# Kernel tuning notes

Hardware: AMD Instinct MI355X
Metric: run time of the kernel (lower is better)

## Reference

```python
import math
import jax, jax.numpy as jnp
import numpy as np

N_HEADS = 16


def setup_inputs() -> dict:
    key = jax.random.key(0)
    k1, k2 = jax.random.split(key)
    qkv = jax.random.normal(k1, (2, 3072, 2048), dtype=jnp.float32)
    mask = jax.random.randint(k2, (2, 1, 2048), 0, 2).astype(jnp.bool_)
    return {"qkv": qkv, "mask": mask}


def reference(qkv, mask):
    bs, width, length = qkv.shape
    ch = width // (3 * N_HEADS)
    q, k, v = jnp.split(qkv, 3, axis=1)  # each [bs, H*C, T]
    scale = 1.0 / math.sqrt(math.sqrt(ch))  # applied to both q and k
    q = (q * scale).reshape(bs * N_HEADS, ch, length)
    k = (k * scale).reshape(bs * N_HEADS, ch, length)
    # [B*H, T, T] scores
    weight = jnp.einsum('bct,bcs->bts', q, k)
    # mask: [bs, 1, T] bool, True = valid token
    inv = ~mask[:, 0, :]                      # [bs, T]
    pad = inv[:, None, :] | inv[:, :, None]   # [bs, T, T]
    pad = jnp.broadcast_to(pad[:, None], (bs, N_HEADS, length, length))
    pad = pad.reshape(bs * N_HEADS, length, length)
    weight = jnp.where(pad, jnp.finfo(weight.dtype).min, weight)
    weight = jax.nn.softmax(weight.astype(jnp.float32), axis=-1).astype(qkv.dtype)
    a = jnp.einsum('bts,bcs->bct', weight, v.reshape(bs * N_HEADS, ch, length))
    return a.reshape(bs, N_HEADS * ch, length)
```

## Files before the change

kernel.cpp:

```cpp
#include <hip/hip_runtime.h>
#include <float.h>


typedef __attribute__((ext_vector_type(8))) short bf16x8;
typedef __attribute__((ext_vector_type(4))) float f32x4;

#define TSEQ 2048
#define QT_OFF 0L
#define KF_OFF 4194304L
#define VF_OFF 8388608L

#if __has_builtin(__builtin_amdgcn_exp2f)
#define EXPFN(x) __builtin_amdgcn_exp2f(x)
#define SM_SCALE (0.125f * 1.44269504088896f)
#else
#define EXPFN(x) __expf(x)
#define SM_SCALE 0.125f
#endif

__device__ inline short f2bf(float x) {
    union { float f; unsigned u; } un; un.f = x;
    unsigned r = un.u + 0x7fffu + ((un.u >> 16) & 1u);
    return (short)(r >> 16);
}

__device__ inline unsigned pkbf(float a, float b) {
    unsigned au = __float_as_uint(a) + 0x8000u;
    unsigned bu = __float_as_uint(b) + 0x8000u;
    return __builtin_amdgcn_perm(bu, au, 0x07060302u);
}

__global__ __launch_bounds__(256) void prep_kernel(
    const float* __restrict__ qkv, short* __restrict__ ws)
{
    const int tid = threadIdx.x;
    const int job = blockIdx.x;
    if (job < 2048) {
        __shared__ float Ls[64 * 65];
        const int which = job & 1;
        const int rest  = job >> 1;
        const int bh = rest & 31, tt = rest >> 5;
        const int b = bh >> 4, h = bh & 15;
        const float* src = qkv + (long)b * 6291456 + ((long)(which * 1024 + h * 64)) * TSEQ + tt * 64;
        #pragma unroll
        for (int ch = 0; ch < 4; ++ch) {
            int idx = tid + ch * 256;
            int c = idx >> 4, tch = idx & 15;
            float4 v = *(const float4*)(src + (long)c * TSEQ + tch * 4);
            float* L = &Ls[c * 65 + tch * 4];
            L[0] = v.x; L[1] = v.y; L[2] = v.z; L[3] = v.w;
        }
        __syncthreads();
        if (which == 0) {
            short* dst = ws + QT_OFF + ((long)bh * TSEQ + tt * 64) * 64;
            #pragma unroll
            for (int ch = 0; ch < 2; ++ch) {
                int idx = tid + ch * 256;
                int t = idx >> 3, cch = idx & 7;
                bf16x8 o;
                #pragma unroll
                for (int j = 0; j < 8; ++j)
                    o[j] = f2bf(Ls[(cch * 8 + j) * 65 + t] * SM_SCALE);
                *(bf16x8*)(dst + (long)t * 64 + cch * 8) = o;
            }
        } else {
            short* dst = ws + KF_OFF + (long)(bh * 32 + tt) * 4096;
            #pragma unroll
            for (int ch = 0; ch < 2; ++ch) {
                int u = tid + ch * 256;
                int f = u >> 6, lane = u & 63;
                int q = lane >> 4, l15 = lane & 15;
                int hf = f & 1, ns = f >> 1;
                bf16x8 o;
                #pragma unroll
                for (int j = 0; j < 8; ++j)
                    o[j] = f2bf(Ls[(hf * 32 + q * 8 + j) * 65 + ns * 16 + l15]);
                *(bf16x8*)(dst + f * 512 + lane * 8) = o;
            }
        }
    } else {
        const int v = job - 2048;
        const int head = v >> 5, it = v & 31;
        const int b = head >> 4, h = head & 15;
        short* dst = ws + VF_OFF + (long)(head * 32 + it) * 4096;
        #pragma unroll
        for (int ch = 0; ch < 2; ++ch) {
            int u = tid * 2 + ch;
            int f = u >> 6, lane = u & 63;
            int q = lane >> 4, l15 = lane & 15;
            int hf = f & 1, nc = f >> 1;
            const float* src = qkv + (long)b * 6291456
                + ((long)(2048 + h * 64 + nc * 16 + l15)) * TSEQ
                + it * 64 + hf * 32 + q * 8;
            float4 a  = *(const float4*)src;
            float4 c4 = *(const float4*)(src + 4);
            bf16x8 o;
            o[0] = f2bf(a.x);  o[1] = f2bf(a.y);  o[2] = f2bf(a.z);  o[3] = f2bf(a.w);
            o[4] = f2bf(c4.x); o[5] = f2bf(c4.y); o[6] = f2bf(c4.z); o[7] = f2bf(c4.w);
            *(bf16x8*)(dst + f * 512 + lane * 8) = o;
        }
    }
}

__global__ __launch_bounds__(512, 2) void attn_kernel(
    const short* __restrict__ ws, const int* __restrict__ mask,
    float* __restrict__ out)
{
    __shared__ __align__(16) char smem[66560];
    short* Ps  = (short*)smem;
    float* mbf = (float*)(smem + 32768);
    float* Os  = (float*)smem;

    const int tid  = threadIdx.x;
    const int lane = tid & 63, wid = tid >> 6;
    const int l15  = lane & 15, quad = lane >> 4;

    const int blk  = blockIdx.x;
    const int head = blk & 31;
    const int qt   = blk >> 5;
    const int b    = head >> 4, h = head & 15;
    const int t0   = qt * 256;

    const short* QT = ws + QT_OFF + (long)head * 131072;
    const short* KF = ws + KF_OFF + (long)head * 131072;
    const short* VF = ws + VF_OFF + (long)head * 131072;
    const long obase = ((long)b * 1024 + h * 64) * TSEQ;

    for (int i = tid; i < TSEQ; i += 512)
        mbf[i] = (mask[b * TSEQ + i] != 0) ? 0.0f : -1e30f;
    __syncthreads();

    bf16x8 qb[2][2];
    #pragma unroll
    for (int nt = 0; nt < 2; ++nt)
        #pragma unroll
        for (int hf = 0; hf < 2; ++hf)
            qb[nt][hf] = *(const bf16x8*)(QT +
                (long)(t0 + wid * 32 + nt * 16 + l15) * 64 + quad * 8 + hf * 32);
    bool qv[2];
    #pragma unroll
    for (int nt = 0; nt < 2; ++nt)
        qv[nt] = (mbf[t0 + wid * 32 + nt * 16 + l15] != 0.0f);

    float l_s[2] = {0.0f, 0.0f};
    f32x4 Oacc[2][4];
    #pragma unroll
    for (int mt = 0; mt < 2; ++mt)
        #pragma unroll
        for (int nc = 0; nc < 4; ++nc)
            #pragma unroll
            for (int r = 0; r < 4; ++r) Oacc[mt][nc][r] = 0.0f;

    short* Pw = Ps + wid * 2048;

    bf16x8 kc[8];
    #pragma unroll
    for (int f = 0; f < 8; ++f)
        kc[f] = *(const bf16x8*)(KF + (long)f * 512 + lane * 8);

    for (int it = 0; it < 32; ++it) {
        const int itn = (it + 1) & 31;

        bf16x8 vf[8];
        #pragma unroll
        for (int f = 0; f < 8; ++f)
            vf[f] = *(const bf16x8*)(VF + ((long)it * 8 + f) * 512 + lane * 8);
        bf16x8 kn[8];
        #pragma unroll
        for (int f = 0; f < 8; ++f)
            kn[f] = *(const bf16x8*)(KF + ((long)itn * 8 + f) * 512 + lane * 8);

        f32x4 bias[4];
        #pragma unroll
        for (int ns = 0; ns < 4; ++ns)
            bias[ns] = *(const f32x4*)&mbf[it * 64 + ns * 16 + quad * 4];

        f32x4 Sacc[4][2];
        #pragma unroll
        for (int ns = 0; ns < 4; ++ns)
            #pragma unroll
            for (int nt = 0; nt < 2; ++nt) {
                Sacc[ns][nt] = __builtin_amdgcn_mfma_f32_16x16x32_bf16(
                    kc[ns * 2 + 0], qb[nt][0], bias[ns], 0, 0, 0);
                Sacc[ns][nt] = __builtin_amdgcn_mfma_f32_16x16x32_bf16(
                    kc[ns * 2 + 1], qb[nt][1], Sacc[ns][nt], 0, 0, 0);
            }

        #pragma unroll
        for (int nt = 0; nt < 2; ++nt) {
            const int row = nt * 16 + l15;
            const int sw  = (row & 7) ^ ((row & 8) >> 1);
            float ls = 0.0f;
            #pragma unroll
            for (int ns = 0; ns < 4; ++ns) {
                float pv[4];
                #pragma unroll
                for (int r = 0; r < 4; ++r) {
                    float e = EXPFN(Sacc[ns][nt][r]);
                    pv[r] = qv[nt] ? 1.0f : e;
                    ls += pv[r];
                }
                const int cbp = (ns * 2 + (quad >> 1)) ^ sw;
                uint2 pk;
                pk.x = pkbf(pv[0], pv[1]);
                pk.y = pkbf(pv[2], pv[3]);
                *(uint2*)&Pw[row * 64 + cbp * 8 + (quad & 1) * 4] = pk;
            }
            ls += __shfl_xor(ls, 16);
            ls += __shfl_xor(ls, 32);
            l_s[nt] += ls;
        }

        bf16x8 pa[2][2];
        #pragma unroll
        for (int mt = 0; mt < 2; ++mt) {
            const int row = mt * 16 + l15;
            const int sw  = (row & 7) ^ ((row & 8) >> 1);
            #pragma unroll
            for (int hf = 0; hf < 2; ++hf)
                pa[mt][hf] = *(const bf16x8*)&Pw[row * 64 + ((quad + 4 * hf) ^ sw) * 8];
        }
        #pragma unroll
        for (int hf = 0; hf < 2; ++hf)
            #pragma unroll
            for (int nc = 0; nc < 4; ++nc)
                #pragma unroll
                for (int mt = 0; mt < 2; ++mt)
                    Oacc[mt][nc] = __builtin_amdgcn_mfma_f32_16x16x32_bf16(
                        pa[mt][hf], vf[nc * 2 + hf], Oacc[mt][nc], 0, 0, 0);

        #pragma unroll
        for (int f = 0; f < 8; ++f) kc[f] = kn[f];
    }

    __syncthreads();
    float inv[2];
    #pragma unroll
    for (int nt = 0; nt < 2; ++nt) inv[nt] = 1.0f / l_s[nt];
    float iw[2][4];
    #pragma unroll
    for (int mt = 0; mt < 2; ++mt)
        #pragma unroll
        for (int r = 0; r < 4; ++r)
            iw[mt][r] = __shfl(inv[mt], 4 * quad + r);
    #pragma unroll
    for (int mt = 0; mt < 2; ++mt)
        #pragma unroll
        for (int nc = 0; nc < 4; ++nc) {
            float4 o;
            o.x = Oacc[mt][nc][0] * iw[mt][0];
            o.y = Oacc[mt][nc][1] * iw[mt][1];
            o.z = Oacc[mt][nc][2] * iw[mt][2];
            o.w = Oacc[mt][nc][3] * iw[mt][3];
            *(float4*)&Os[(nc * 16 + l15) * 260 + wid * 32 + mt * 16 + quad * 4] = o;
        }
    __syncthreads();
    #pragma unroll
    for (int ch = 0; ch < 8; ++ch) {
        int idx = tid + ch * 512;
        int c = idx >> 6, tch = idx & 63;
        *(float4*)(out + obase + (long)c * TSEQ + t0 + tch * 4) =
            *(const float4*)&Os[c * 260 + tch * 4];
    }
}

extern "C" void kernel_launch(void* const* d_in, const int* in_sizes, int n_in,
                              void* d_out, int out_size, void* d_ws, size_t ws_size,
                              hipStream_t stream) {
    const float* qkv  = (const float*)d_in[0];
    const int*   mask = (const int*)d_in[1];
    float*       out  = (float*)d_out;
    short*       ws   = (short*)d_ws;
    prep_kernel<<<dim3(3072), dim3(256), 0, stream>>>(qkv, ws);
    attn_kernel<<<dim3(256), dim3(512), 0, stream>>>(ws, mask, out);
}
```

Baseline: 142.7 us.

## Stage K/V tiles in shared double-buffered LDS via global_load_lds

Until now every wave loaded the full K and V tiles for each iteration straight from global memory into registers, so the same data was fetched eight times per block. Now each wave issues one 16-byte global_load_lds per K and V tile into a double-buffered LDS region that all waves share. The next tile is prefetched while the current one is consumed, and waves read their fragments from LDS. MFMA sections are also wrapped in s_setprio to favour matrix issue. The trade-off is a block-wide barrier every iteration and more LDS per block (73728 bytes), which could limit overlap between waves.

```diff
diff --git a/kernel.cpp b/kernel.cpp
--- a/kernel.cpp
+++ b/kernel.cpp
@@ -17,6 +17,10 @@
 #define EXPFN(x) __expf(x)
 #define SM_SCALE 0.125f
 #endif
+
+#define GLOAD16(g, l) __builtin_amdgcn_global_load_lds( \
+    (const __attribute__((address_space(1))) void*)(g), \
+    (__attribute__((address_space(3))) void*)(l), 16, 0, 0)
 
 __device__ inline short f2bf(float x) {
     union { float f; unsigned u; } un; un.f = x;
@@ -106,9 +110,9 @@
     const short* __restrict__ ws, const int* __restrict__ mask,
     float* __restrict__ out)
 {
-    __shared__ __align__(16) char smem[66560];
-    short* Ps  = (short*)smem;
-    float* mbf = (float*)(smem + 32768);
+    __shared__ __align__(16) char smem[73728];
+    short* Ps  = (short*)(smem + 32768);
+    float* mbf = (float*)(smem + 65536);
     float* Os  = (float*)smem;
 
     const int tid  = threadIdx.x;
@@ -122,12 +126,15 @@
     const int t0   = qt * 256;
 
     const short* QT = ws + QT_OFF + (long)head * 131072;
-    const short* KF = ws + KF_OFF + (long)head * 131072;
-    const short* VF = ws + VF_OFF + (long)head * 131072;
+    const char*  KB = (const char*)(ws + KF_OFF + (long)head * 131072);
+    const char*  VB = (const char*)(ws + VF_OFF + (long)head * 131072);
     const long obase = ((long)b * 1024 + h * 64) * TSEQ;
 
     for (int i = tid; i < TSEQ; i += 512)
         mbf[i] = (mask[b * TSEQ + i] != 0) ? 0.0f : -1e30f;
+
+    GLOAD16(KB + wid * 1024 + lane * 16, smem + wid * 1024);
+    GLOAD16(VB + wid * 1024 + lane * 16, smem + 8192 + wid * 1024);
     __syncthreads();
 
     bf16x8 qb[2][2];
@@ -153,22 +160,22 @@
 
     short* Pw = Ps + wid * 2048;
 
-    bf16x8 kc[8];
-    #pragma unroll
-    for (int f = 0; f < 8; ++f)
-        kc[f] = *(const bf16x8*)(KF + (long)f * 512 + lane * 8);
-
+    int cur = 0;
     for (int it = 0; it < 32; ++it) {
-        const int itn = (it + 1) & 31;
-
-        bf16x8 vf[8];
+        if (it != 31) {
+            const long nb = (long)(it + 1) * 8192;
+            GLOAD16(KB + nb + wid * 1024 + lane * 16,
+                    smem + (cur ^ 1) * 16384 + wid * 1024);
+            GLOAD16(VB + nb + wid * 1024 + lane * 16,
+                    smem + (cur ^ 1) * 16384 + 8192 + wid * 1024);
+        }
+        const short* kb = (const short*)(smem + cur * 16384);
+        const short* vb = (const short*)(smem + cur * 16384 + 8192);
+
+        bf16x8 kc[8];
         #pragma unroll
         for (int f = 0; f < 8; ++f)
-            vf[f] = *(const bf16x8*)(VF + ((long)it * 8 + f) * 512 + lane * 8);
-        bf16x8 kn[8];
-        #pragma unroll
-        for (int f = 0; f < 8; ++f)
-            kn[f] = *(const bf16x8*)(KF + ((long)itn * 8 + f) * 512 + lane * 8);
+            kc[f] = *(const bf16x8*)(kb + f * 512 + lane * 8);
 
         f32x4 bias[4];
         #pragma unroll
@@ -176,6 +183,7 @@
             bias[ns] = *(const f32x4*)&mbf[it * 64 + ns * 16 + quad * 4];
 
         f32x4 Sacc[4][2];
+        __builtin_amdgcn_s_setprio(1);
         #pragma unroll
         for (int ns = 0; ns < 4; ++ns)
             #pragma unroll
@@ -185,6 +193,7 @@
                 Sacc[ns][nt] = __builtin_amdgcn_mfma_f32_16x16x32_bf16(
                     kc[ns * 2 + 1], qb[nt][1], Sacc[ns][nt], 0, 0, 0);
             }
+        __builtin_amdgcn_s_setprio(0);
 
         #pragma unroll
         for (int nt = 0; nt < 2; ++nt) {
@@ -220,6 +229,12 @@
             for (int hf = 0; hf < 2; ++hf)
                 pa[mt][hf] = *(const bf16x8*)&Pw[row * 64 + ((quad + 4 * hf) ^ sw) * 8];
         }
+        bf16x8 vf[8];
+        #pragma unroll
+        for (int f = 0; f < 8; ++f)
+            vf[f] = *(const bf16x8*)(vb + f * 512 + lane * 8);
+
+        __builtin_amdgcn_s_setprio(1);
         #pragma unroll
         for (int hf = 0; hf < 2; ++hf)
             #pragma unroll
@@ -228,12 +243,12 @@
                 for (int mt = 0; mt < 2; ++mt)
                     Oacc[mt][nc] = __builtin_amdgcn_mfma_f32_16x16x32_bf16(
                         pa[mt][hf], vf[nc * 2 + hf], Oacc[mt][nc], 0, 0, 0);
-
-        #pragma unroll
-        for (int f = 0; f < 8; ++f) kc[f] = kn[f];
+        __builtin_amdgcn_s_setprio(0);
+
+        __syncthreads();
+        cur ^= 1;
     }
 
-    __syncthreads();
     float inv[2];
     #pragma unroll
     for (int nt = 0; nt < 2; ++nt) inv[nt] = 1.0f / l_s[nt];
```

Result: slower. 148.1 us (+3.8%).

## Split key sequence across wave pairs with smaller query tiles for more blocks

Applied to the files above, without the earlier changes.

The attention kernel now uses 64-query tiles with 256-thread blocks (1024 blocks instead of 256). Each pair of waves processes interleaved halves of the key tiles, and the partial row sums and outputs are combined through shared memory at the end. The K prefetch pipeline is removed, V loads move after the softmax, and s_setprio wraps the MFMA sections. The prep kernel's V write mapping also changes. The aim is better CU occupancy and load balance on a 256-CU part, at the cost of an extra reduction step and less software prefetching.

```diff
diff --git a/kernel.cpp b/kernel.cpp
--- a/kernel.cpp
+++ b/kernel.cpp
@@ -85,7 +85,7 @@
         short* dst = ws + VF_OFF + (long)(head * 32 + it) * 4096;
         #pragma unroll
         for (int ch = 0; ch < 2; ++ch) {
-            int u = tid * 2 + ch;
+            int u = tid + ch * 256;
             int f = u >> 6, lane = u & 63;
             int q = lane >> 4, l15 = lane & 15;
             int hf = f & 1, nc = f >> 1;
@@ -102,31 +102,33 @@
     }
 }
 
-__global__ __launch_bounds__(512, 2) void attn_kernel(
-    const short* __restrict__ ws, const int* __restrict__ mask,
+__global__ __launch_bounds__(256, 4) void attn_kernel(
+    const short* __restrict__ wsp, const int* __restrict__ mask,
     float* __restrict__ out)
 {
-    __shared__ __align__(16) char smem[66560];
+    __shared__ __align__(16) char smem[24576];
     short* Ps  = (short*)smem;
-    float* mbf = (float*)(smem + 32768);
+    float* mbf = (float*)(smem + 16384);
     float* Os  = (float*)smem;
+    float* Lc  = (float*)(smem + 20480);
 
     const int tid  = threadIdx.x;
     const int lane = tid & 63, wid = tid >> 6;
     const int l15  = lane & 15, quad = lane >> 4;
+    const int wq   = wid & 1,  wss  = wid >> 1;
 
     const int blk  = blockIdx.x;
     const int head = blk & 31;
     const int qt   = blk >> 5;
     const int b    = head >> 4, h = head & 15;
-    const int t0   = qt * 256;
-
-    const short* QT = ws + QT_OFF + (long)head * 131072;
-    const short* KF = ws + KF_OFF + (long)head * 131072;
-    const short* VF = ws + VF_OFF + (long)head * 131072;
+    const int t0   = qt * 64;
+
+    const short* QT = wsp + QT_OFF + (long)head * 131072;
+    const short* KF = wsp + KF_OFF + (long)head * 131072;
+    const short* VF = wsp + VF_OFF + (long)head * 131072;
     const long obase = ((long)b * 1024 + h * 64) * TSEQ;
 
-    for (int i = tid; i < TSEQ; i += 512)
+    for (int i = tid; i < TSEQ; i += 256)
         mbf[i] = (mask[b * TSEQ + i] != 0) ? 0.0f : -1e30f;
     __syncthreads();
 
@@ -136,11 +138,11 @@
         #pragma unroll
         for (int hf = 0; hf < 2; ++hf)
             qb[nt][hf] = *(const bf16x8*)(QT +
-                (long)(t0 + wid * 32 + nt * 16 + l15) * 64 + quad * 8 + hf * 32);
+                (long)(t0 + wq * 32 + nt * 16 + l15) * 64 + quad * 8 + hf * 32);
     bool qv[2];
     #pragma unroll
     for (int nt = 0; nt < 2; ++nt)
-        qv[nt] = (mbf[t0 + wid * 32 + nt * 16 + l15] != 0.0f);
+        qv[nt] = (mbf[t0 + wq * 32 + nt * 16 + l15] != 0.0f);
 
     float l_s[2] = {0.0f, 0.0f};
     f32x4 Oacc[2][4];
@@ -152,23 +154,17 @@
             for (int r = 0; r < 4; ++r) Oacc[mt][nc][r] = 0.0f;
 
     short* Pw = Ps + wid * 2048;
-
-    bf16x8 kc[8];
-    #pragma unroll
-    for (int f = 0; f < 8; ++f)
-        kc[f] = *(const bf16x8*)(KF + (long)f * 512 + lane * 8);
-
-    for (int it = 0; it < 32; ++it) {
-        const int itn = (it + 1) & 31;
-
-        bf16x8 vf[8];
+    const short* KL = KF + lane * 8;
+    const short* VL = VF + lane * 8;
+
+    for (int i = 0; i < 16; ++i) {
+        const int it = wss + i * 2;
+
+        const short* kp = KL + (long)it * 4096;
+        bf16x8 kc[8];
         #pragma unroll
         for (int f = 0; f < 8; ++f)
-            vf[f] = *(const bf16x8*)(VF + ((long)it * 8 + f) * 512 + lane * 8);
-        bf16x8 kn[8];
-        #pragma unroll
-        for (int f = 0; f < 8; ++f)
-            kn[f] = *(const bf16x8*)(KF + ((long)itn * 8 + f) * 512 + lane * 8);
+            kc[f] = *(const bf16x8*)(kp + f * 512);
 
         f32x4 bias[4];
         #pragma unroll
@@ -176,6 +172,7 @@
             bias[ns] = *(const f32x4*)&mbf[it * 64 + ns * 16 + quad * 4];
 
         f32x4 Sacc[4][2];
+        __builtin_amdgcn_s_setprio(1);
         #pragma unroll
         for (int ns = 0; ns < 4; ++ns)
             #pragma unroll
@@ -185,6 +182,7 @@
                 Sacc[ns][nt] = __builtin_amdgcn_mfma_f32_16x16x32_bf16(
                     kc[ns * 2 + 1], qb[nt][1], Sacc[ns][nt], 0, 0, 0);
             }
+        __builtin_amdgcn_s_setprio(0);
 
         #pragma unroll
         for (int nt = 0; nt < 2; ++nt) {
@@ -211,6 +209,12 @@
             l_s[nt] += ls;
         }
 
+        const short* vp = VL + (long)it * 4096;
+        bf16x8 vf[8];
+        #pragma unroll
+        for (int f = 0; f < 8; ++f)
+            vf[f] = *(const bf16x8*)(vp + f * 512);
+
         bf16x8 pa[2][2];
         #pragma unroll
         for (int mt = 0; mt < 2; ++mt) {
@@ -220,6 +224,7 @@
             for (int hf = 0; hf < 2; ++hf)
                 pa[mt][hf] = *(const bf16x8*)&Pw[row * 64 + ((quad + 4 * hf) ^ sw) * 8];
         }
+        __builtin_amdgcn_s_setprio(1);
         #pragma unroll
         for (int hf = 0; hf < 2; ++hf)
             #pragma unroll
@@ -228,39 +233,59 @@
                 for (int mt = 0; mt < 2; ++mt)
                     Oacc[mt][nc] = __builtin_amdgcn_mfma_f32_16x16x32_bf16(
                         pa[mt][hf], vf[nc * 2 + hf], Oacc[mt][nc], 0, 0, 0);
-
-        #pragma unroll
-        for (int f = 0; f < 8; ++f) kc[f] = kn[f];
-    }
-
+        __builtin_amdgcn_s_setprio(0);
+    }
+
+    __syncthreads();
+    if (quad == 0) {
+        Lc[wid * 32 + l15]      = l_s[0];
+        Lc[wid * 32 + 16 + l15] = l_s[1];
+    }
     __syncthreads();
     float inv[2];
     #pragma unroll
-    for (int nt = 0; nt < 2; ++nt) inv[nt] = 1.0f / l_s[nt];
+    for (int nt = 0; nt < 2; ++nt)
+        inv[nt] = 1.0f / (l_s[nt] + Lc[(wid ^ 2) * 32 + nt * 16 + l15]);
     float iw[2][4];
     #pragma unroll
     for (int mt = 0; mt < 2; ++mt)
         #pragma unroll
         for (int r = 0; r < 4; ++r)
             iw[mt][r] = __shfl(inv[mt], 4 * quad + r);
-    #pragma unroll
-    for (int mt = 0; mt < 2; ++mt)
-        #pragma unroll
-        for (int nc = 0; nc < 4; ++nc) {
-            float4 o;
-            o.x = Oacc[mt][nc][0] * iw[mt][0];
-            o.y = Oacc[mt][nc][1] * iw[mt][1];
-            o.z = Oacc[mt][nc][2] * iw[mt][2];
-            o.w = Oacc[mt][nc][3] * iw[mt][3];
-            *(float4*)&Os[(nc * 16 + l15) * 260 + wid * 32 + mt * 16 + quad * 4] = o;
-        }
-    __syncthreads();
-    #pragma unroll
-    for (int ch = 0; ch < 8; ++ch) {
-        int idx = tid + ch * 512;
-        int c = idx >> 6, tch = idx & 63;
+
+    if (wss == 0) {
+        #pragma unroll
+        for (int mt = 0; mt < 2; ++mt)
+            #pragma unroll
+            for (int nc = 0; nc < 4; ++nc) {
+                float4 o;
+                o.x = Oacc[mt][nc][0] * iw[mt][0];
+                o.y = Oacc[mt][nc][1] * iw[mt][1];
+                o.z = Oacc[mt][nc][2] * iw[mt][2];
+                o.w = Oacc[mt][nc][3] * iw[mt][3];
+                *(float4*)&Os[(nc * 16 + l15) * 68 + wq * 32 + mt * 16 + quad * 4] = o;
+            }
+    }
+    __syncthreads();
+    if (wss == 1) {
+        #pragma unroll
+        for (int mt = 0; mt < 2; ++mt)
+            #pragma unroll
+            for (int nc = 0; nc < 4; ++nc) {
+                float* p = &Os[(nc * 16 + l15) * 68 + wq * 32 + mt * 16 + quad * 4];
+                p[0] += Oacc[mt][nc][0] * iw[mt][0];
+                p[1] += Oacc[mt][nc][1] * iw[mt][1];
+                p[2] += Oacc[mt][nc][2] * iw[mt][2];
+                p[3] += Oacc[mt][nc][3] * iw[mt][3];
+            }
+    }
+    __syncthreads();
+    #pragma unroll
+    for (int ch = 0; ch < 4; ++ch) {
+        int idx = tid + ch * 256;
+        int c = idx >> 4, tch = idx & 15;
         *(float4*)(out + obase + (long)c * TSEQ + t0 + tch * 4) =
-            *(const float4*)&Os[c * 260 + tch * 4];
+            *(const float4*)&Os[c * 68 + tch * 4];
     }
 }
 
@@ -272,5 +297,5 @@
     float*       out  = (float*)d_out;
     short*       ws   = (short*)d_ws;
     prep_kernel<<<dim3(3072), dim3(256), 0, stream>>>(qkv, ws);
-    attn_kernel<<<dim3(256), dim3(512), 0, stream>>>(ws, mask, out);
-}
+    attn_kernel<<<dim3(1024), dim3(256), 0, stream>>>(ws, mask, out);
+}
```

After: 137.0 us. 4.1% less time.
